# Optimization experiments

Hardware: AMD Instinct MI355X
Metric: run time of the kernel (lower is better)

Reference implementation:

```python
import jax, jax.numpy as jnp
import numpy as np

B, L = 256, 128            # batch_size, max_len
VOCAB, EMB = 50000, 448
POS_NUM, POS_SZ = 128, 32
UNITS = 512                # gru_units == EMB + 2*POS_SZ (BiGRU input dim)
NUM_CLASSES = 53


def setup_inputs() -> dict:
    key = jax.random.key(0)
    ks = jax.random.split(key, 16)
    s = 0.05
    return {
        "input_word": jax.random.randint(ks[0], (B, L), 0, VOCAB),
        "input_pos1": jax.random.randint(ks[1], (B, L), 0, POS_NUM),
        "input_pos2": jax.random.randint(ks[2], (B, L), 0, POS_NUM),
        "word_emb": jax.random.normal(ks[3], (VOCAB, EMB), jnp.float32) * s,
        "pos_emb": jax.random.normal(ks[4], (POS_NUM, POS_SZ), jnp.float32) * s,
        # Keras GRU (reset_after=True): kernel [D,3U], recurrent_kernel [U,3U], bias [2,3U]
        "gru_kernel_f": jax.random.normal(ks[5], (UNITS, 3 * UNITS), jnp.float32) * s,
        "gru_rkernel_f": jax.random.normal(ks[6], (UNITS, 3 * UNITS), jnp.float32) * s,
        "gru_bias_f": jax.random.normal(ks[7], (2, 3 * UNITS), jnp.float32) * s,
        "gru_kernel_b": jax.random.normal(ks[8], (UNITS, 3 * UNITS), jnp.float32) * s,
        "gru_rkernel_b": jax.random.normal(ks[9], (UNITS, 3 * UNITS), jnp.float32) * s,
        "gru_bias_b": jax.random.normal(ks[10], (2, 3 * UNITS), jnp.float32) * s,
        "attention_w": jax.random.normal(ks[11], (UNITS, 1), jnp.float32) * s,
        "sen_a": jax.random.normal(ks[12], (UNITS,), jnp.float32) * s,
        "sen_r": jax.random.normal(ks[13], (UNITS, 1), jnp.float32) * s,
        "sen_d": jax.random.normal(ks[14], (NUM_CLASSES,), jnp.float32) * s,
        "sen_s": jax.random.normal(ks[15], (NUM_CLASSES, UNITS), jnp.float32) * s,
    }


def _gru(x, kernel, rkernel, bias):
    """Keras GRU, reset_after=True, tanh/sigmoid activations. x: [B,L,D] -> [B,L,U]."""
    bi, br = bias[0], bias[1]
    # precompute input projections for all timesteps: [B,L,3U]
    xp = jnp.einsum('bld,dh->blh', x, kernel) + bi
    U = rkernel.shape[0]
    def step(h, xt):  # xt: [B,3U]
        rec = h @ rkernel + br
        xz, xr, xh = jnp.split(xt, 3, axis=-1)
        rz, rr, rh = jnp.split(rec, 3, axis=-1)
        z = jax.nn.sigmoid(xz + rz)
        r = jax.nn.sigmoid(xr + rr)
        hh = jnp.tanh(xh + r * rh)
        h_new = z * h + (1.0 - z) * hh
        return h_new, h_new
    h0 = jnp.zeros((x.shape[0], U), x.dtype)
    _, hs = jax.lax.scan(step, h0, jnp.swapaxes(xp, 0, 1))  # [L,B,U]
    return jnp.swapaxes(hs, 0, 1)


def _bigru(x, kf, rf, bf, kb, rb, bb):
    """Bidirectional GRU, merge_mode='sum'."""
    fwd = _gru(x, kf, rf, bf)
    bwd = _gru(x[:, ::-1], kb, rb, bb)[:, ::-1]
    return fwd + bwd


def reference(input_word, input_pos1, input_pos2, word_emb, pos_emb,
              gru_kernel_f, gru_rkernel_f, gru_bias_f,
              gru_kernel_b, gru_rkernel_b, gru_bias_b,
              attention_w, sen_a, sen_r, sen_d, sen_s):
    # embedding lookups; embedding of reversed indices == time-reverse of embedding
    we = word_emb[input_word]        # [B,L,EMB]
    p1 = pos_emb[input_pos1]         # [B,L,POS_SZ]
    p2 = pos_emb[input_pos2]
    x_f = jnp.concatenate([we, p1, p2], axis=-1)  # [B,L,UNITS]
    x_b = x_f[:, ::-1]
    # same BiGRU (shared weights) applied to forward and reversed inputs, summed
    h = (_bigru(x_f, gru_kernel_f, gru_rkernel_f, gru_bias_f,
                gru_kernel_b, gru_rkernel_b, gru_bias_b)
         + _bigru(x_b, gru_kernel_f, gru_rkernel_f, gru_bias_f,
                  gru_kernel_b, gru_rkernel_b, gru_bias_b))  # dropout = identity (inference)
    inputs_h = jnp.tanh(h)  # [B,L,U]
    # word attention: scalar score per token, softmax over sequence
    scores = (inputs_h @ attention_w)[..., 0]           # [B,L]
    w_alpha = jax.nn.softmax(scores, axis=-1)           # [B,L]
    w_att_r = jnp.einsum('bl,blu->bu', w_alpha, h)      # weighted sum of PRE-tanh h
    # sentence attention (vectorized over what was a per-sample Python loop)
    r = jnp.tanh(w_att_r)                               # [B,U]
    e = ((r * sen_a) @ sen_r)[:, 0]                     # [B]
    a = jax.nn.softmax(e, axis=0)[:, None]              # softmax across the batch, [B,1]
    s_c = a * r                                         # [B,U]
    logits = s_c @ sen_s.T + sen_d                      # [B,C]
    return jax.nn.softmax(logits, axis=-1)
```

## Files before the change

kernel.cpp:

```cpp
#include <hip/hip_runtime.h>
#include <cstddef>
#include <cstdint>

#define BATCH 256
#define SEQL  128
#define BL    (BATCH * SEQL)
#define DIM   512
#define N3    1536
#define NCLS  53

typedef float f32x4 __attribute__((ext_vector_type(4)));
typedef short s16x8 __attribute__((ext_vector_type(8)));

__device__ __forceinline__ float bf2f(unsigned short u) {
    union { unsigned int i; float f; } v; v.i = ((unsigned int)u) << 16; return v.f;
}
__device__ __forceinline__ unsigned short f2bf(float f) {
    union { float f; unsigned int i; } v; v.f = f;
    unsigned int x = v.i;
    return (unsigned short)((x + 0x7fffu + ((x >> 16) & 1u)) >> 16);
}
__device__ __forceinline__ float wave_sum(float v) {
    #pragma unroll
    for (int m = 32; m > 0; m >>= 1) v += __shfl_xor(v, m);
    return v;
}
__device__ __forceinline__ float wave_max(float v) {
    #pragma unroll
    for (int m = 32; m > 0; m >>= 1) v = fmaxf(v, __shfl_xor(v, m));
    return v;
}
__device__ __forceinline__ float sigmoidf(float x) { return 1.0f / (1.0f + expf(-x)); }

__global__ __launch_bounds__(256) void zero_state_kernel(float* Hf, unsigned short* Hb) {
    int i = blockIdx.x * 256 + threadIdx.x;
    Hf[i] = 0.0f;
    Hb[i] = 0;
}

__global__ __launch_bounds__(256) void transpose_kernel(const float* __restrict__ W,
                                                        unsigned short* __restrict__ Wt) {
    __shared__ float tile[32][33];
    int tx = threadIdx.x & 31, ty = threadIdx.x >> 5;
    int n0 = blockIdx.x * 32, k0 = blockIdx.y * 32;
    #pragma unroll
    for (int r = 0; r < 4; ++r) {
        int kl = ty + r * 8;
        tile[kl][tx] = W[(size_t)(k0 + kl) * N3 + n0 + tx];
    }
    __syncthreads();
    #pragma unroll
    for (int r = 0; r < 4; ++r) {
        int nl = ty + r * 8;
        Wt[(size_t)(n0 + nl) * DIM + k0 + tx] = f2bf(tile[tx][nl]);
    }
}

__global__ __launch_bounds__(64) void gather_kernel(const int* __restrict__ iw,
                                                    const int* __restrict__ ip1,
                                                    const int* __restrict__ ip2,
                                                    const float* __restrict__ wemb,
                                                    const float* __restrict__ pemb,
                                                    unsigned short* __restrict__ X) {
    int row = blockIdx.x;
    int tid = threadIdx.x;
    int w = iw[row], p1 = ip1[row], p2 = ip2[row];
    int e0 = tid * 8;
    s16x8 o;
    #pragma unroll
    for (int j = 0; j < 8; ++j) {
        int e = e0 + j;
        float f;
        if (e < 448)      f = wemb[(size_t)w * 448 + e];
        else if (e < 480) f = pemb[p1 * 32 + (e - 448)];
        else              f = pemb[p2 * 32 + (e - 480)];
        o[j] = (short)f2bf(f);
    }
    *(s16x8*)(X + (size_t)row * DIM + e0) = o;
}

__global__ __launch_bounds__(256, 2) void xp_gemm_kernel(const unsigned short* __restrict__ X,
                                                         const unsigned short* __restrict__ Ktf,
                                                         const unsigned short* __restrict__ Ktb,
                                                         unsigned short* __restrict__ XPf,
                                                         unsigned short* __restrict__ XPb) {
    const unsigned short* Kt = blockIdx.z ? Ktb : Ktf;
    unsigned short* XP = blockIdx.z ? XPb : XPf;
    int row0 = blockIdx.x * 64;
    int n0   = blockIdx.y * 256;

    __shared__ alignas(16) unsigned short As[64 * 512];
    int tid = threadIdx.x;
    const char* src = (const char*)(X + (size_t)row0 * DIM);
    #pragma unroll
    for (int i = 0; i < 16; ++i) {
        int lin = (tid + i * 256) * 16;
        int row = lin >> 10;
        int swz = lin ^ ((row & 7) << 4);
        *(s16x8*)((char*)As + swz) = *(const s16x8*)(src + lin);
    }
    __syncthreads();

    int lane = tid & 63, wv = tid >> 6;
    int wr = wv >> 1, wc = wv & 1;
    int lr = lane & 15, lk = (lane >> 4) * 8;

    f32x4 acc[2][8];
    #pragma unroll
    for (int mi = 0; mi < 2; ++mi)
        #pragma unroll
        for (int ni = 0; ni < 8; ++ni) acc[mi][ni] = (f32x4){0.f, 0.f, 0.f, 0.f};

    int r0 = wr * 32 + lr, r1 = r0 + 16;
    const unsigned short* bp = Kt + (size_t)(n0 + wc * 128 + lr) * DIM + lk;

    for (int kk = 0; kk < 16; ++kk) {
        int kb = kk * 64 + lk * 2;
        s16x8 a0 = *(const s16x8*)((const char*)As + ((r0 * 1024 + kb) ^ ((r0 & 7) << 4)));
        s16x8 a1 = *(const s16x8*)((const char*)As + ((r1 * 1024 + kb) ^ ((r1 & 7) << 4)));
        #pragma unroll
        for (int ni = 0; ni < 8; ++ni) {
            s16x8 b = *(const s16x8*)(bp + (size_t)ni * 16 * DIM + kk * 32);
            acc[0][ni] = __builtin_amdgcn_mfma_f32_16x16x32_bf16(a0, b, acc[0][ni], 0, 0, 0);
            acc[1][ni] = __builtin_amdgcn_mfma_f32_16x16x32_bf16(a1, b, acc[1][ni], 0, 0, 0);
        }
    }

    int rbase = (lane >> 4) * 4;
    #pragma unroll
    for (int mi = 0; mi < 2; ++mi) {
        #pragma unroll
        for (int ni = 0; ni < 8; ++ni) {
            int n = n0 + wc * 128 + ni * 16 + lr;
            #pragma unroll
            for (int reg = 0; reg < 4; ++reg) {
                int gr = row0 + wr * 32 + mi * 16 + rbase + reg;
                int b = gr >> 7, l = gr & 127;
                XP[((size_t)l * 256 + b) * N3 + n] = f2bf(acc[mi][ni][reg]);
            }
        }
    }
}

__global__ __launch_bounds__(256, 2) void gru_step2_kernel(
    const unsigned short* __restrict__ Hb_in, const float* __restrict__ Hf_in,
    unsigned short* __restrict__ Hb_out, float* __restrict__ Hf_out,
    const unsigned short* __restrict__ XPf, const unsigned short* __restrict__ XPb,
    const unsigned short* __restrict__ Btf, const unsigned short* __restrict__ Btb,
    const float* __restrict__ gbf, const float* __restrict__ gbb,
    unsigned short* __restrict__ H1, unsigned short* __restrict__ H2, int t) {
    int row0 = blockIdx.x * 32;
    int u0   = blockIdx.y * 32;
    int runidx = blockIdx.x >> 3;

    const unsigned short* Bt = (runidx < 2) ? Btf : Btb;
    const float* gb = (runidx < 2) ? gbf : gbb;
    const float* bi  = gb;
    const float* brp = gb + N3;
    int tx = (runidx == 1 || runidx == 2) ? (127 - t) : t;
    int th = (runidx >= 2) ? (127 - t) : t;
    unsigned short* Hdst = (runidx & 1) ? H2 : H1;
    const unsigned short* xps = ((runidx < 2) ? XPf : XPb) + (size_t)tx * 256 * N3;

    __shared__ alignas(16) unsigned short As[32 * 512];
    int tid = threadIdx.x;
    const char* src = (const char*)(Hb_in + (size_t)row0 * DIM);
    #pragma unroll
    for (int i = 0; i < 8; ++i) {
        int lin = (tid + i * 256) * 16;
        int row = lin >> 10;
        int swz = lin ^ ((row & 7) << 4);
        *(s16x8*)((char*)As + swz) = *(const s16x8*)(src + lin);
    }
    __syncthreads();

    int lane = tid & 63, wv = tid >> 6;
    int wr = wv >> 1, wc = wv & 1;
    int lr = lane & 15, lk = (lane >> 4) * 8;

    f32x4 aZ = (f32x4){0.f, 0.f, 0.f, 0.f};
    f32x4 aR = (f32x4){0.f, 0.f, 0.f, 0.f};
    f32x4 aH = (f32x4){0.f, 0.f, 0.f, 0.f};

    int ar = wr * 16 + lr;
    const unsigned short* bp = Bt + (size_t)(u0 + wc * 16 + lr) * DIM + lk;

    for (int kk = 0; kk < 16; ++kk) {
        int kb = kk * 64 + lk * 2;
        s16x8 af = *(const s16x8*)((const char*)As + ((ar * 1024 + kb) ^ ((ar & 7) << 4)));
        s16x8 bz = *(const s16x8*)(bp + kk * 32);
        s16x8 br = *(const s16x8*)(bp + (size_t)512 * DIM + kk * 32);
        s16x8 bh = *(const s16x8*)(bp + (size_t)1024 * DIM + kk * 32);
        aZ = __builtin_amdgcn_mfma_f32_16x16x32_bf16(af, bz, aZ, 0, 0, 0);
        aR = __builtin_amdgcn_mfma_f32_16x16x32_bf16(af, br, aR, 0, 0, 0);
        aH = __builtin_amdgcn_mfma_f32_16x16x32_bf16(af, bh, aH, 0, 0, 0);
    }

    int cu = u0 + wc * 16 + lr;
    float biz = bi[cu], bir = bi[512 + cu], bih = bi[1024 + cu];
    float brz = brp[cu], brr = brp[512 + cu], brh = brp[1024 + cu];
    int rbase = (lane >> 4) * 4;
    #pragma unroll
    for (int reg = 0; reg < 4; ++reg) {
        int row = row0 + wr * 16 + rbase + reg;
        int b = row & 255;
        const unsigned short* xpp = xps + (size_t)b * N3 + cu;
        float xz = bf2f(xpp[0]), xr = bf2f(xpp[512]), xh = bf2f(xpp[1024]);
        float z  = sigmoidf(xz + biz + aZ[reg] + brz);
        float rg = sigmoidf(xr + bir + aR[reg] + brr);
        float hh = tanhf(xh + bih + rg * (aH[reg] + brh));
        float hp = Hf_in[(size_t)row * DIM + cu];
        float hn = z * hp + (1.0f - z) * hh;
        Hf_out[(size_t)row * DIM + cu] = hn;
        unsigned short hb = f2bf(hn);
        Hb_out[(size_t)row * DIM + cu] = hb;
        Hdst[((size_t)b * SEQL + th) * DIM + cu] = hb;
    }
}

__global__ __launch_bounds__(64) void attn_scores_kernel(const unsigned short* __restrict__ H1,
                                                         const unsigned short* __restrict__ H2,
                                                         const float* __restrict__ attw,
                                                         float* __restrict__ scores) {
    int bl = blockIdx.x;
    int lane = threadIdx.x;
    size_t base = (size_t)bl * DIM + lane * 8;
    s16x8 h1 = *(const s16x8*)(H1 + base);
    s16x8 h2 = *(const s16x8*)(H2 + base);
    float s = 0.0f;
    #pragma unroll
    for (int j = 0; j < 8; ++j) {
        float hv = bf2f((unsigned short)h1[j]) + bf2f((unsigned short)h2[j]);
        s += tanhf(hv) * attw[lane * 8 + j];
    }
    s = wave_sum(s);
    if (lane == 0) scores[bl] = s;
}

__global__ __launch_bounds__(64) void softmax_l_kernel(const float* __restrict__ scores,
                                                       float* __restrict__ alpha) {
    int b = blockIdx.x, lane = threadIdx.x;
    float s0 = scores[b * SEQL + lane];
    float s1 = scores[b * SEQL + 64 + lane];
    float m = wave_max(fmaxf(s0, s1));
    float e0 = expf(s0 - m), e1 = expf(s1 - m);
    float sum = wave_sum(e0 + e1);
    alpha[b * SEQL + lane] = e0 / sum;
    alpha[b * SEQL + 64 + lane] = e1 / sum;
}

__global__ __launch_bounds__(256) void attn_apply_kernel(const unsigned short* __restrict__ H1,
                                                         const unsigned short* __restrict__ H2,
                                                         const float* __restrict__ alpha,
                                                         const float* __restrict__ sena,
                                                         const float* __restrict__ senr,
                                                         float* __restrict__ rbuf,
                                                         float* __restrict__ ebuf) {
    int b = blockIdx.x, tid = threadIdx.x;
    __shared__ float al[SEQL];
    __shared__ float red[4];
    if (tid < SEQL) al[tid] = alpha[b * SEQL + tid];
    __syncthreads();
    float w0 = 0.0f, w1 = 0.0f;
    for (int l = 0; l < SEQL; ++l) {
        size_t base = ((size_t)b * SEQL + l) * DIM;
        float a = al[l];
        w0 += a * (bf2f(H1[base + tid]) + bf2f(H2[base + tid]));
        w1 += a * (bf2f(H1[base + 256 + tid]) + bf2f(H2[base + 256 + tid]));
    }
    float r0 = tanhf(w0), r1 = tanhf(w1);
    rbuf[(size_t)b * DIM + tid] = r0;
    rbuf[(size_t)b * DIM + 256 + tid] = r1;
    float p = r0 * sena[tid] * senr[tid] + r1 * sena[256 + tid] * senr[256 + tid];
    p = wave_sum(p);
    int wid = tid >> 6;
    if ((tid & 63) == 0) red[wid] = p;
    __syncthreads();
    if (tid == 0) ebuf[b] = red[0] + red[1] + red[2] + red[3];
}

__global__ __launch_bounds__(64) void batch_softmax_kernel(const float* __restrict__ ebuf,
                                                           float* __restrict__ abuf) {
    int lane = threadIdx.x;
    float v0 = ebuf[lane], v1 = ebuf[64 + lane], v2 = ebuf[128 + lane], v3 = ebuf[192 + lane];
    float m = wave_max(fmaxf(fmaxf(v0, v1), fmaxf(v2, v3)));
    float e0 = expf(v0 - m), e1 = expf(v1 - m), e2 = expf(v2 - m), e3 = expf(v3 - m);
    float s = wave_sum(e0 + e1 + e2 + e3);
    abuf[lane] = e0 / s; abuf[64 + lane] = e1 / s;
    abuf[128 + lane] = e2 / s; abuf[192 + lane] = e3 / s;
}

__global__ __launch_bounds__(64) void final_out_kernel(const float* __restrict__ rbuf,
                                                       const float* __restrict__ abuf,
                                                       const float* __restrict__ sens,
                                                       const float* __restrict__ send,
                                                       float* __restrict__ out) {
    int b = blockIdx.x, lane = threadIdx.x;
    __shared__ float lg[NCLS];
    float ab = abuf[b];
    float rv[8];
    #pragma unroll
    for (int j = 0; j < 8; ++j) rv[j] = rbuf[(size_t)b * DIM + j * 64 + lane];
    for (int c = 0; c < NCLS; ++c) {
        float d = 0.0f;
        #pragma unroll
        for (int j = 0; j < 8; ++j) d += rv[j] * sens[(size_t)c * DIM + j * 64 + lane];
        d = wave_sum(d);
        if (lane == 0) lg[c] = ab * d + send[c];
    }
    __syncthreads();
    float x = (lane < NCLS) ? lg[lane] : -3.0e38f;
    float m = wave_max(x);
    float ex = (lane < NCLS) ? expf(x - m) : 0.0f;
    float s = wave_sum(ex);
    if (lane < NCLS) out[b * NCLS + lane] = ex / s;
}

extern "C" void kernel_launch(void* const* d_in, const int* in_sizes, int n_in,
                              void* d_out, int out_size, void* d_ws, size_t ws_size,
                              hipStream_t stream) {
    (void)in_sizes; (void)n_in; (void)out_size; (void)ws_size;
    const int*   iw   = (const int*)d_in[0];
    const int*   ip1  = (const int*)d_in[1];
    const int*   ip2  = (const int*)d_in[2];
    const float* wemb = (const float*)d_in[3];
    const float* pemb = (const float*)d_in[4];
    const float* kf   = (const float*)d_in[5];
    const float* rf   = (const float*)d_in[6];
    const float* gbf  = (const float*)d_in[7];
    const float* kb   = (const float*)d_in[8];
    const float* rb   = (const float*)d_in[9];
    const float* gbb  = (const float*)d_in[10];
    const float* attw = (const float*)d_in[11];
    const float* sena = (const float*)d_in[12];
    const float* senr = (const float*)d_in[13];
    const float* send = (const float*)d_in[14];
    const float* sens = (const float*)d_in[15];
    float* out = (float*)d_out;

    char* p = (char*)d_ws;
    auto take = [&](size_t n) { char* q = p; p += ((n + 255) & ~(size_t)255); return q; };
    unsigned short* X    = (unsigned short*)take((size_t)BL * DIM * 2);
    unsigned short* Ktf  = (unsigned short*)take((size_t)N3 * DIM * 2);
    unsigned short* Ktb  = (unsigned short*)take((size_t)N3 * DIM * 2);
    unsigned short* Btf  = (unsigned short*)take((size_t)N3 * DIM * 2);
    unsigned short* Btb  = (unsigned short*)take((size_t)N3 * DIM * 2);
    float*          Hf0  = (float*)take((size_t)1024 * DIM * 4);
    float*          Hf1  = (float*)take((size_t)1024 * DIM * 4);
    unsigned short* Hb0  = (unsigned short*)take((size_t)1024 * DIM * 2);
    unsigned short* Hb1  = (unsigned short*)take((size_t)1024 * DIM * 2);
    unsigned short* XPf  = (unsigned short*)take((size_t)BL * N3 * 2);
    unsigned short* XPb  = (unsigned short*)take((size_t)BL * N3 * 2);
    unsigned short* H1   = (unsigned short*)take((size_t)BL * DIM * 2);
    unsigned short* H2   = (unsigned short*)take((size_t)BL * DIM * 2);
    float* scores = (float*)take((size_t)BL * 4);
    float* alpha  = (float*)take((size_t)BL * 4);
    float* rbuf   = (float*)take((size_t)BATCH * DIM * 4);
    float* ebuf   = (float*)take((size_t)BATCH * 4);
    float* abuf   = (float*)take((size_t)BATCH * 4);

    zero_state_kernel<<<2048, 256, 0, stream>>>(Hf0, Hb0);
    transpose_kernel<<<dim3(48, 16), 256, 0, stream>>>(kf, Ktf);
    transpose_kernel<<<dim3(48, 16), 256, 0, stream>>>(kb, Ktb);
    transpose_kernel<<<dim3(48, 16), 256, 0, stream>>>(rf, Btf);
    transpose_kernel<<<dim3(48, 16), 256, 0, stream>>>(rb, Btb);
    gather_kernel<<<BL, 64, 0, stream>>>(iw, ip1, ip2, wemb, pemb, X);

    xp_gemm_kernel<<<dim3(512, 6, 2), 256, 0, stream>>>(X, Ktf, Ktb, XPf, XPb);

    for (int t = 0; t < SEQL; ++t) {
        const unsigned short* hbi; const float* hfi;
        unsigned short* hbo; float* hfo;
        if (t & 1) { hbi = Hb1; hfi = Hf1; hbo = Hb0; hfo = Hf0; }
        else       { hbi = Hb0; hfi = Hf0; hbo = Hb1; hfo = Hf1; }
        gru_step2_kernel<<<dim3(32, 16), 256, 0, stream>>>(
            hbi, hfi, hbo, hfo, XPf, XPb, Btf, Btb, gbf, gbb, H1, H2, t);
    }

    attn_scores_kernel<<<BL, 64, 0, stream>>>(H1, H2, attw, scores);
    softmax_l_kernel<<<BATCH, 64, 0, stream>>>(scores, alpha);
    attn_apply_kernel<<<BATCH, 256, 0, stream>>>(H1, H2, alpha, sena, senr, rbuf, ebuf);
    batch_softmax_kernel<<<1, 64, 0, stream>>>(ebuf, abuf);
    final_out_kernel<<<BATCH, 64, 0, stream>>>(rbuf, abuf, sens, send, out);
}
```

Baseline: 2.536 ms.

## Replace per-timestep GRU launches with one persistent scan kernel

Replaces the 128 per-timestep GRU kernel launches with one persistent kernel: 32 workgroups, each owning a 32-row batch block of one run, loop over all timesteps. Hidden state stays in double-buffered shared memory and fp32 registers, and workgroups synchronise with block barriers instead of kernel boundaries. The input-projection GEMM now writes its output in the fragment layout the scan kernel reads, so each lane loads its gate inputs contiguously. This removes launch overhead and global round trips of the hidden state, but only 32 workgroups are active during the scan, so most of the GPU sits idle and recurrent weights are reread from cache every step.

```diff
diff --git a/kernel.cpp b/kernel.cpp
--- a/kernel.cpp
+++ b/kernel.cpp
@@ -11,6 +11,7 @@
 
 typedef float f32x4 __attribute__((ext_vector_type(4)));
 typedef short s16x8 __attribute__((ext_vector_type(8)));
+typedef short s16x4 __attribute__((ext_vector_type(4)));
 
 __device__ __forceinline__ float bf2f(unsigned short u) {
     union { unsigned int i; float f; } v; v.i = ((unsigned int)u) << 16; return v.f;
@@ -31,12 +32,6 @@
     return v;
 }
 __device__ __forceinline__ float sigmoidf(float x) { return 1.0f / (1.0f + expf(-x)); }
-
-__global__ __launch_bounds__(256) void zero_state_kernel(float* Hf, unsigned short* Hb) {
-    int i = blockIdx.x * 256 + threadIdx.x;
-    Hf[i] = 0.0f;
-    Hb[i] = 0;
-}
 
 __global__ __launch_bounds__(256) void transpose_kernel(const float* __restrict__ W,
                                                         unsigned short* __restrict__ Wt) {
@@ -79,158 +74,230 @@
     *(s16x8*)(X + (size_t)row * DIM + e0) = o;
 }
 
-__global__ __launch_bounds__(256, 2) void xp_gemm_kernel(const unsigned short* __restrict__ X,
+__global__ __launch_bounds__(256, 2) void xq_gemm_kernel(const unsigned short* __restrict__ X,
                                                          const unsigned short* __restrict__ Ktf,
                                                          const unsigned short* __restrict__ Ktb,
-                                                         unsigned short* __restrict__ XPf,
-                                                         unsigned short* __restrict__ XPb) {
-    const unsigned short* Kt = blockIdx.z ? Ktb : Ktf;
-    unsigned short* XP = blockIdx.z ? XPb : XPf;
-    int row0 = blockIdx.x * 64;
-    int n0   = blockIdx.y * 256;
+                                                         unsigned short* __restrict__ XQf,
+                                                         unsigned short* __restrict__ XQb) {
+    int dir = blockIdx.z & 1;
+    int ns  = blockIdx.z >> 1;
+    const unsigned short* Kt = dir ? Ktb : Ktf;
+    unsigned short* XQ = dir ? XQb : XQf;
+    int bblk = blockIdx.y;
+    int b0 = bblk * 32;
+    int l0 = blockIdx.x * 2;
+    int u0 = ns * 128;
 
     __shared__ alignas(16) unsigned short As[64 * 512];
     int tid = threadIdx.x;
-    const char* src = (const char*)(X + (size_t)row0 * DIM);
-    #pragma unroll
-    for (int i = 0; i < 16; ++i) {
-        int lin = (tid + i * 256) * 16;
+    #pragma unroll
+    for (int it = 0; it < 16; ++it) {
+        int lin = (it * 256 + tid) * 16;
         int row = lin >> 10;
-        int swz = lin ^ ((row & 7) << 4);
-        *(s16x8*)((char*)As + swz) = *(const s16x8*)(src + lin);
+        int off = lin & 1023;
+        int i = row & 31, j = row >> 5;
+        const char* src = (const char*)X + ((((size_t)(b0 + i)) * 128 + (size_t)(l0 + j)) << 10) + off;
+        *(s16x8*)((char*)As + (lin ^ ((row & 7) << 4))) = *(const s16x8*)src;
     }
     __syncthreads();
 
     int lane = tid & 63, wv = tid >> 6;
-    int wr = wv >> 1, wc = wv & 1;
-    int lr = lane & 15, lk = (lane >> 4) * 8;
-
-    f32x4 acc[2][8];
+    int lr = lane & 15, lg = lane >> 4;
+
+    f32x4 acc[3][8];
+    #pragma unroll
+    for (int g = 0; g < 3; ++g)
+        #pragma unroll
+        for (int nii = 0; nii < 8; ++nii) acc[g][nii] = (f32x4){0.f, 0.f, 0.f, 0.f};
+
+    int ar = wv * 16 + lr;
+    for (int kk = 0; kk < 16; ++kk) {
+        s16x8 a = *(const s16x8*)((const char*)As +
+                    (((ar << 10) + (kk << 6) + (lg << 4)) ^ ((ar & 7) << 4)));
+        #pragma unroll
+        for (int g = 0; g < 3; ++g)
+            #pragma unroll
+            for (int nii = 0; nii < 8; ++nii) {
+                const unsigned short* bp = Kt + ((size_t)(g * 512 + u0 + nii * 16 + lr) << 9)
+                                              + (kk << 5) + (lg << 3);
+                s16x8 b = *(const s16x8*)bp;
+                acc[g][nii] = __builtin_amdgcn_mfma_f32_16x16x32_bf16(a, b, acc[g][nii], 0, 0, 0);
+            }
+    }
+
+    int txo = l0 + (wv >> 1);
+    int mi_t = wv & 1;
+    #pragma unroll
+    for (int g = 0; g < 3; ++g)
+        #pragma unroll
+        for (int nii = 0; nii < 8; ++nii) {
+            int w_t  = ns * 2 + (nii >> 2);
+            int ni_t = nii & 3;
+            size_t base = (((size_t)txo * 8 + bblk) * 8 + w_t) * 6144
+                        + (size_t)(((g * 4 + ni_t) * 2 + mi_t)) * 256;
+            s16x4 o;
+            #pragma unroll
+            for (int reg = 0; reg < 4; ++reg) o[reg] = (short)f2bf(acc[g][nii][reg]);
+            *(s16x4*)(XQ + base + lane * 4) = o;
+        }
+}
+
+__global__ __launch_bounds__(512, 2) void gru_scan_kernel(
+    const unsigned short* __restrict__ XQf, const unsigned short* __restrict__ XQb,
+    const unsigned short* __restrict__ Btf, const unsigned short* __restrict__ Btb,
+    const float* __restrict__ gbf, const float* __restrict__ gbb,
+    unsigned short* __restrict__ HA, unsigned short* __restrict__ HB,
+    unsigned short* __restrict__ HC, unsigned short* __restrict__ HD) {
+    int wg = blockIdx.x;
+    int runidx = wg >> 3;
+    int bblk = wg & 7;
+    int b0 = bblk * 32;
+    const unsigned short* Bt = (runidx < 2) ? Btf : Btb;
+    const unsigned short* XQ = (runidx < 2) ? XQf : XQb;
+    const float* gb = (runidx < 2) ? gbf : gbb;
+    unsigned short* Hout = (runidx == 0) ? HA : (runidx == 1) ? HB : (runidx == 2) ? HC : HD;
+    bool revx = (runidx == 1 || runidx == 2);
+    bool revo = (runidx >= 2);
+
+    int tid = threadIdx.x;
+    int lane = tid & 63, w = tid >> 6;
+    int lr = lane & 15, lg = lane >> 4;
+    int u0 = w * 64;
+
+    __shared__ alignas(16) unsigned short Hs[2][32 * 512];
+
+    {
+        s16x8 z8 = (s16x8){0, 0, 0, 0, 0, 0, 0, 0};
+        #pragma unroll
+        for (int i = 0; i < 4; ++i) ((s16x8*)Hs[0])[tid + i * 512] = z8;
+    }
+
+    float bZ[4], bR[4], bIH[4], bRH[4];
+    #pragma unroll
+    for (int ni = 0; ni < 4; ++ni) {
+        int n = u0 + ni * 16 + lr;
+        bZ[ni]  = gb[n] + gb[N3 + n];
+        bR[ni]  = gb[512 + n] + gb[N3 + 512 + n];
+        bIH[ni] = gb[1024 + n];
+        bRH[ni] = gb[N3 + 1024 + n];
+    }
+
+    f32x4 hf[2][4];
     #pragma unroll
     for (int mi = 0; mi < 2; ++mi)
         #pragma unroll
-        for (int ni = 0; ni < 8; ++ni) acc[mi][ni] = (f32x4){0.f, 0.f, 0.f, 0.f};
-
-    int r0 = wr * 32 + lr, r1 = r0 + 16;
-    const unsigned short* bp = Kt + (size_t)(n0 + wc * 128 + lr) * DIM + lk;
-
-    for (int kk = 0; kk < 16; ++kk) {
-        int kb = kk * 64 + lk * 2;
-        s16x8 a0 = *(const s16x8*)((const char*)As + ((r0 * 1024 + kb) ^ ((r0 & 7) << 4)));
-        s16x8 a1 = *(const s16x8*)((const char*)As + ((r1 * 1024 + kb) ^ ((r1 & 7) << 4)));
-        #pragma unroll
-        for (int ni = 0; ni < 8; ++ni) {
-            s16x8 b = *(const s16x8*)(bp + (size_t)ni * 16 * DIM + kk * 32);
-            acc[0][ni] = __builtin_amdgcn_mfma_f32_16x16x32_bf16(a0, b, acc[0][ni], 0, 0, 0);
-            acc[1][ni] = __builtin_amdgcn_mfma_f32_16x16x32_bf16(a1, b, acc[1][ni], 0, 0, 0);
-        }
-    }
-
-    int rbase = (lane >> 4) * 4;
-    #pragma unroll
-    for (int mi = 0; mi < 2; ++mi) {
-        #pragma unroll
-        for (int ni = 0; ni < 8; ++ni) {
-            int n = n0 + wc * 128 + ni * 16 + lr;
-            #pragma unroll
-            for (int reg = 0; reg < 4; ++reg) {
-                int gr = row0 + wr * 32 + mi * 16 + rbase + reg;
-                int b = gr >> 7, l = gr & 127;
-                XP[((size_t)l * 256 + b) * N3 + n] = f2bf(acc[mi][ni][reg]);
+        for (int ni = 0; ni < 4; ++ni) hf[mi][ni] = (f32x4){0.f, 0.f, 0.f, 0.f};
+
+    __syncthreads();
+
+    for (int t = 0; t < SEQL; ++t) {
+        int cur = t & 1;
+        int tx = revx ? (127 - t) : t;
+        int th = revo ? (127 - t) : t;
+
+        const unsigned short* xqb = XQ + (((size_t)tx * 8 + bblk) * 8 + w) * 6144 + (size_t)lane * 4;
+        s16x4 xq[3][4][2];
+        #pragma unroll
+        for (int g = 0; g < 3; ++g)
+            #pragma unroll
+            for (int ni = 0; ni < 4; ++ni)
+                #pragma unroll
+                for (int mi = 0; mi < 2; ++mi)
+                    xq[g][ni][mi] = *(const s16x4*)(xqb + ((g * 4 + ni) * 2 + mi) * 256);
+
+        const char* hs = (const char*)Hs[cur];
+        int r0 = lr, r1 = 16 + lr;
+
+        f32x4 aZ[2][4], aR[2][4];
+        #pragma unroll
+        for (int mi = 0; mi < 2; ++mi)
+            #pragma unroll
+            for (int ni = 0; ni < 4; ++ni) {
+                aZ[mi][ni] = (f32x4){0.f, 0.f, 0.f, 0.f};
+                aR[mi][ni] = (f32x4){0.f, 0.f, 0.f, 0.f};
+            }
+        for (int kk = 0; kk < 16; ++kk) {
+            s16x8 a0 = *(const s16x8*)(hs + (((r0 << 10) + (kk << 6) + (lg << 4)) ^ ((r0 & 7) << 4)));
+            s16x8 a1 = *(const s16x8*)(hs + (((r1 << 10) + (kk << 6) + (lg << 4)) ^ ((r1 & 7) << 4)));
+            #pragma unroll
+            for (int ni = 0; ni < 4; ++ni) {
+                const unsigned short* bp = Bt + ((size_t)(u0 + ni * 16 + lr) << 9) + (kk << 5) + (lg << 3);
+                s16x8 bz = *(const s16x8*)bp;
+                s16x8 br = *(const s16x8*)(bp + (512 << 9));
+                aZ[0][ni] = __builtin_amdgcn_mfma_f32_16x16x32_bf16(a0, bz, aZ[0][ni], 0, 0, 0);
+                aZ[1][ni] = __builtin_amdgcn_mfma_f32_16x16x32_bf16(a1, bz, aZ[1][ni], 0, 0, 0);
+                aR[0][ni] = __builtin_amdgcn_mfma_f32_16x16x32_bf16(a0, br, aR[0][ni], 0, 0, 0);
+                aR[1][ni] = __builtin_amdgcn_mfma_f32_16x16x32_bf16(a1, br, aR[1][ni], 0, 0, 0);
             }
         }
-    }
-}
-
-__global__ __launch_bounds__(256, 2) void gru_step2_kernel(
-    const unsigned short* __restrict__ Hb_in, const float* __restrict__ Hf_in,
-    unsigned short* __restrict__ Hb_out, float* __restrict__ Hf_out,
-    const unsigned short* __restrict__ XPf, const unsigned short* __restrict__ XPb,
-    const unsigned short* __restrict__ Btf, const unsigned short* __restrict__ Btb,
-    const float* __restrict__ gbf, const float* __restrict__ gbb,
-    unsigned short* __restrict__ H1, unsigned short* __restrict__ H2, int t) {
-    int row0 = blockIdx.x * 32;
-    int u0   = blockIdx.y * 32;
-    int runidx = blockIdx.x >> 3;
-
-    const unsigned short* Bt = (runidx < 2) ? Btf : Btb;
-    const float* gb = (runidx < 2) ? gbf : gbb;
-    const float* bi  = gb;
-    const float* brp = gb + N3;
-    int tx = (runidx == 1 || runidx == 2) ? (127 - t) : t;
-    int th = (runidx >= 2) ? (127 - t) : t;
-    unsigned short* Hdst = (runidx & 1) ? H2 : H1;
-    const unsigned short* xps = ((runidx < 2) ? XPf : XPb) + (size_t)tx * 256 * N3;
-
-    __shared__ alignas(16) unsigned short As[32 * 512];
-    int tid = threadIdx.x;
-    const char* src = (const char*)(Hb_in + (size_t)row0 * DIM);
-    #pragma unroll
-    for (int i = 0; i < 8; ++i) {
-        int lin = (tid + i * 256) * 16;
-        int row = lin >> 10;
-        int swz = lin ^ ((row & 7) << 4);
-        *(s16x8*)((char*)As + swz) = *(const s16x8*)(src + lin);
-    }
-    __syncthreads();
-
-    int lane = tid & 63, wv = tid >> 6;
-    int wr = wv >> 1, wc = wv & 1;
-    int lr = lane & 15, lk = (lane >> 4) * 8;
-
-    f32x4 aZ = (f32x4){0.f, 0.f, 0.f, 0.f};
-    f32x4 aR = (f32x4){0.f, 0.f, 0.f, 0.f};
-    f32x4 aH = (f32x4){0.f, 0.f, 0.f, 0.f};
-
-    int ar = wr * 16 + lr;
-    const unsigned short* bp = Bt + (size_t)(u0 + wc * 16 + lr) * DIM + lk;
-
-    for (int kk = 0; kk < 16; ++kk) {
-        int kb = kk * 64 + lk * 2;
-        s16x8 af = *(const s16x8*)((const char*)As + ((ar * 1024 + kb) ^ ((ar & 7) << 4)));
-        s16x8 bz = *(const s16x8*)(bp + kk * 32);
-        s16x8 br = *(const s16x8*)(bp + (size_t)512 * DIM + kk * 32);
-        s16x8 bh = *(const s16x8*)(bp + (size_t)1024 * DIM + kk * 32);
-        aZ = __builtin_amdgcn_mfma_f32_16x16x32_bf16(af, bz, aZ, 0, 0, 0);
-        aR = __builtin_amdgcn_mfma_f32_16x16x32_bf16(af, br, aR, 0, 0, 0);
-        aH = __builtin_amdgcn_mfma_f32_16x16x32_bf16(af, bh, aH, 0, 0, 0);
-    }
-
-    int cu = u0 + wc * 16 + lr;
-    float biz = bi[cu], bir = bi[512 + cu], bih = bi[1024 + cu];
-    float brz = brp[cu], brr = brp[512 + cu], brh = brp[1024 + cu];
-    int rbase = (lane >> 4) * 4;
-    #pragma unroll
-    for (int reg = 0; reg < 4; ++reg) {
-        int row = row0 + wr * 16 + rbase + reg;
-        int b = row & 255;
-        const unsigned short* xpp = xps + (size_t)b * N3 + cu;
-        float xz = bf2f(xpp[0]), xr = bf2f(xpp[512]), xh = bf2f(xpp[1024]);
-        float z  = sigmoidf(xz + biz + aZ[reg] + brz);
-        float rg = sigmoidf(xr + bir + aR[reg] + brr);
-        float hh = tanhf(xh + bih + rg * (aH[reg] + brh));
-        float hp = Hf_in[(size_t)row * DIM + cu];
-        float hn = z * hp + (1.0f - z) * hh;
-        Hf_out[(size_t)row * DIM + cu] = hn;
-        unsigned short hb = f2bf(hn);
-        Hb_out[(size_t)row * DIM + cu] = hb;
-        Hdst[((size_t)b * SEQL + th) * DIM + cu] = hb;
-    }
-}
-
-__global__ __launch_bounds__(64) void attn_scores_kernel(const unsigned short* __restrict__ H1,
-                                                         const unsigned short* __restrict__ H2,
+        #pragma unroll
+        for (int mi = 0; mi < 2; ++mi)
+            #pragma unroll
+            for (int ni = 0; ni < 4; ++ni)
+                #pragma unroll
+                for (int reg = 0; reg < 4; ++reg) {
+                    aZ[mi][ni][reg] = sigmoidf(bf2f((unsigned short)xq[0][ni][mi][reg]) + aZ[mi][ni][reg] + bZ[ni]);
+                    aR[mi][ni][reg] = sigmoidf(bf2f((unsigned short)xq[1][ni][mi][reg]) + aR[mi][ni][reg] + bR[ni]);
+                }
+
+        f32x4 aH[2][4];
+        #pragma unroll
+        for (int mi = 0; mi < 2; ++mi)
+            #pragma unroll
+            for (int ni = 0; ni < 4; ++ni) aH[mi][ni] = (f32x4){0.f, 0.f, 0.f, 0.f};
+        for (int kk = 0; kk < 16; ++kk) {
+            s16x8 a0 = *(const s16x8*)(hs + (((r0 << 10) + (kk << 6) + (lg << 4)) ^ ((r0 & 7) << 4)));
+            s16x8 a1 = *(const s16x8*)(hs + (((r1 << 10) + (kk << 6) + (lg << 4)) ^ ((r1 & 7) << 4)));
+            #pragma unroll
+            for (int ni = 0; ni < 4; ++ni) {
+                const unsigned short* bp = Bt + ((size_t)(u0 + ni * 16 + lr) << 9) + (kk << 5) + (lg << 3)
+                                              + ((size_t)1024 << 9);
+                s16x8 bh = *(const s16x8*)bp;
+                aH[0][ni] = __builtin_amdgcn_mfma_f32_16x16x32_bf16(a0, bh, aH[0][ni], 0, 0, 0);
+                aH[1][ni] = __builtin_amdgcn_mfma_f32_16x16x32_bf16(a1, bh, aH[1][ni], 0, 0, 0);
+            }
+        }
+
+        char* hn_lds = (char*)Hs[cur ^ 1];
+        #pragma unroll
+        for (int mi = 0; mi < 2; ++mi)
+            #pragma unroll
+            for (int ni = 0; ni < 4; ++ni)
+                #pragma unroll
+                for (int reg = 0; reg < 4; ++reg) {
+                    int row = mi * 16 + lg * 4 + reg;
+                    int u = u0 + ni * 16 + lr;
+                    float hh = tanhf(bf2f((unsigned short)xq[2][ni][mi][reg]) + bIH[ni]
+                                     + aR[mi][ni][reg] * (aH[mi][ni][reg] + bRH[ni]));
+                    float z = aZ[mi][ni][reg];
+                    float hnv = z * hf[mi][ni][reg] + (1.0f - z) * hh;
+                    hf[mi][ni][reg] = hnv;
+                    unsigned short hb = f2bf(hnv);
+                    *(unsigned short*)(hn_lds + (((row << 10) + (u << 1)) ^ ((row & 7) << 4))) = hb;
+                    Hout[((size_t)(b0 + row) * SEQL + th) * DIM + u] = hb;
+                }
+        __syncthreads();
+    }
+}
+
+__global__ __launch_bounds__(64) void attn_scores_kernel(const unsigned short* __restrict__ HA,
+                                                         const unsigned short* __restrict__ HB,
+                                                         const unsigned short* __restrict__ HC,
+                                                         const unsigned short* __restrict__ HD,
                                                          const float* __restrict__ attw,
                                                          float* __restrict__ scores) {
     int bl = blockIdx.x;
     int lane = threadIdx.x;
     size_t base = (size_t)bl * DIM + lane * 8;
-    s16x8 h1 = *(const s16x8*)(H1 + base);
-    s16x8 h2 = *(const s16x8*)(H2 + base);
+    s16x8 h1 = *(const s16x8*)(HA + base);
+    s16x8 h2 = *(const s16x8*)(HB + base);
+    s16x8 h3 = *(const s16x8*)(HC + base);
+    s16x8 h4 = *(const s16x8*)(HD + base);
     float s = 0.0f;
     #pragma unroll
     for (int j = 0; j < 8; ++j) {
-        float hv = bf2f((unsigned short)h1[j]) + bf2f((unsigned short)h2[j]);
+        float hv = bf2f((unsigned short)h1[j]) + bf2f((unsigned short)h2[j])
+                 + bf2f((unsigned short)h3[j]) + bf2f((unsigned short)h4[j]);
         s += tanhf(hv) * attw[lane * 8 + j];
     }
     s = wave_sum(s);
@@ -249,8 +316,10 @@
     alpha[b * SEQL + 64 + lane] = e1 / sum;
 }
 
-__global__ __launch_bounds__(256) void attn_apply_kernel(const unsigned short* __restrict__ H1,
-                                                         const unsigned short* __restrict__ H2,
+__global__ __launch_bounds__(256) void attn_apply_kernel(const unsigned short* __restrict__ HA,
+                                                         const unsigned short* __restrict__ HB,
+                                                         const unsigned short* __restrict__ HC,
+                                                         const unsigned short* __restrict__ HD,
                                                          const float* __restrict__ alpha,
                                                          const float* __restrict__ sena,
                                                          const float* __restrict__ senr,
@@ -265,8 +334,10 @@
     for (int l = 0; l < SEQL; ++l) {
         size_t base = ((size_t)b * SEQL + l) * DIM;
         float a = al[l];
-        w0 += a * (bf2f(H1[base + tid]) + bf2f(H2[base + tid]));
-        w1 += a * (bf2f(H1[base + 256 + tid]) + bf2f(H2[base + 256 + tid]));
+        w0 += a * (bf2f(HA[base + tid]) + bf2f(HB[base + tid])
+                 + bf2f(HC[base + tid]) + bf2f(HD[base + tid]));
+        w1 += a * (bf2f(HA[base + 256 + tid]) + bf2f(HB[base + 256 + tid])
+                 + bf2f(HC[base + 256 + tid]) + bf2f(HD[base + 256 + tid]));
     }
     float r0 = tanhf(w0), r1 = tanhf(w1);
     rbuf[(size_t)b * DIM + tid] = r0;
@@ -345,41 +416,31 @@
     unsigned short* Ktb  = (unsigned short*)take((size_t)N3 * DIM * 2);
     unsigned short* Btf  = (unsigned short*)take((size_t)N3 * DIM * 2);
     unsigned short* Btb  = (unsigned short*)take((size_t)N3 * DIM * 2);
-    float*          Hf0  = (float*)take((size_t)1024 * DIM * 4);
-    float*          Hf1  = (float*)take((size_t)1024 * DIM * 4);
-    unsigned short* Hb0  = (unsigned short*)take((size_t)1024 * DIM * 2);
-    unsigned short* Hb1  = (unsigned short*)take((size_t)1024 * DIM * 2);
-    unsigned short* XPf  = (unsigned short*)take((size_t)BL * N3 * 2);
-    unsigned short* XPb  = (unsigned short*)take((size_t)BL * N3 * 2);
-    unsigned short* H1   = (unsigned short*)take((size_t)BL * DIM * 2);
-    unsigned short* H2   = (unsigned short*)take((size_t)BL * DIM * 2);
+    unsigned short* XQf  = (unsigned short*)take((size_t)BL * N3 * 2);
+    unsigned short* XQb  = (unsigned short*)take((size_t)BL * N3 * 2);
+    unsigned short* HB   = (unsigned short*)take((size_t)BL * DIM * 2);
+    unsigned short* HC   = (unsigned short*)take((size_t)BL * DIM * 2);
+    unsigned short* HD   = (unsigned short*)take((size_t)BL * DIM * 2);
     float* scores = (float*)take((size_t)BL * 4);
     float* alpha  = (float*)take((size_t)BL * 4);
     float* rbuf   = (float*)take((size_t)BATCH * DIM * 4);
     float* ebuf   = (float*)take((size_t)BATCH * 4);
     float* abuf   = (float*)take((size_t)BATCH * 4);
-
-    zero_state_kernel<<<2048, 256, 0, stream>>>(Hf0, Hb0);
+    unsigned short* HA = X;
+
     transpose_kernel<<<dim3(48, 16), 256, 0, stream>>>(kf, Ktf);
     transpose_kernel<<<dim3(48, 16), 256, 0, stream>>>(kb, Ktb);
     transpose_kernel<<<dim3(48, 16), 256, 0, stream>>>(rf, Btf);
     transpose_kernel<<<dim3(48, 16), 256, 0, stream>>>(rb, Btb);
     gather_kernel<<<BL, 64, 0, stream>>>(iw, ip1, ip2, wemb, pemb, X);
 
-    xp_gemm_kernel<<<dim3(512, 6, 2), 256, 0, stream>>>(X, Ktf, Ktb, XPf, XPb);
-
-    for (int t = 0; t < SEQL; ++t) {
-        const unsigned short* hbi; const float* hfi;
-        unsigned short* hbo; float* hfo;
-        if (t & 1) { hbi = Hb1; hfi = Hf1; hbo = Hb0; hfo = Hf0; }
-        else       { hbi = Hb0; hfi = Hf0; hbo = Hb1; hfo = Hf1; }
-        gru_step2_kernel<<<dim3(32, 16), 256, 0, stream>>>(
-            hbi, hfi, hbo, hfo, XPf, XPb, Btf, Btb, gbf, gbb, H1, H2, t);
-    }
-
-    attn_scores_kernel<<<BL, 64, 0, stream>>>(H1, H2, attw, scores);
+    xq_gemm_kernel<<<dim3(64, 8, 8), 256, 0, stream>>>(X, Ktf, Ktb, XQf, XQb);
+
+    gru_scan_kernel<<<32, 512, 0, stream>>>(XQf, XQb, Btf, Btb, gbf, gbb, HA, HB, HC, HD);
+
+    attn_scores_kernel<<<BL, 64, 0, stream>>>(HA, HB, HC, HD, attw, scores);
     softmax_l_kernel<<<BATCH, 64, 0, stream>>>(scores, alpha);
-    attn_apply_kernel<<<BATCH, 256, 0, stream>>>(H1, H2, alpha, sena, senr, rbuf, ebuf);
+    attn_apply_kernel<<<BATCH, 256, 0, stream>>>(HA, HB, HC, HD, alpha, sena, senr, rbuf, ebuf);
     batch_softmax_kernel<<<1, 64, 0, stream>>>(ebuf, abuf);
     final_out_kernel<<<BATCH, 64, 0, stream>>>(rbuf, abuf, sens, send, out);
 }
```

Measured after the change: 9.160 ms. +261.1%, slower.
